# Kernel optimization log

Measured on AMD Instinct MI355X. Metric: run time of the kernel, lower is better.

Reference implementation:

```python
import jax, jax.numpy as jnp
import numpy as np
import math

NVX = 4096   # vx grid points -> th, vr_vxvy are [NVX, NVX]
NVR = 256    # radial grid points
NL = 2       # max spherical-harmonic degree (original hardcodes n_max=2)
N_LM = (NL + 1) * (NL + 2) // 2  # number of (l, m) pairs with 0<=m<=l<=NL


def _grids():
    vmax_x = 8.0
    dvx = 2.0 * vmax_x / NVX
    vx = jnp.linspace(-vmax_x + dvx / 2, vmax_x - dvx / 2, NVX)
    vmax_r = 8.0 * 1.05 * math.sqrt(2.0)
    dvr = vmax_r / NVR
    vr = jnp.linspace(dvr / 2, vmax_r - dvr / 2, NVR)
    VX, VY = jnp.meshgrid(vx, vx)
    th = jnp.arctan2(VY, VX)
    vr_vxvy = jnp.sqrt(VX ** 2 + VY ** 2)
    return vr.astype(jnp.float32), th.astype(jnp.float32), vr_vxvy.astype(jnp.float32)


def _assoc_legendre(l, m, x):
    """P_l^m(x) with Condon-Shortley phase (matches scipy/jax sph_harm)."""
    pmm = jnp.ones_like(x)
    if m > 0:
        somx2 = jnp.sqrt((1.0 - x) * (1.0 + x))
        fact = 1.0
        for _ in range(m):
            pmm = pmm * (-fact) * somx2
            fact += 2.0
    if l == m:
        return pmm
    pmmp1 = x * (2.0 * m + 1.0) * pmm
    if l == m + 1:
        return pmmp1
    for ll in range(m + 2, l + 1):
        pll = ((2.0 * ll - 1.0) * x * pmmp1 - (ll + m - 1.0) * pmm) / (ll - m)
        pmm, pmmp1 = pmmp1, pll
    return pmmp1


def _ylm_real_theta0(l, m, costh):
    # Re[Y_l^m(theta=0, phi)] = K_lm * P_l^m(cos phi); exp(i*m*0) = 1
    k = math.sqrt((2 * l + 1) / (4.0 * math.pi)
                  * math.factorial(l - m) / math.factorial(l + m))
    return k * _assoc_legendre(l, m, costh)


def setup_inputs() -> dict:
    key = jax.random.key(0)
    # flm stacked row-major over (l, m): (0,0),(1,0),(1,1),(2,0),(2,1),(2,2)
    flm = jax.random.uniform(key, (N_LM, NVR), dtype=jnp.float32)
    vr, th, vr_vxvy = _grids()
    return {"flm": flm, "vr": vr, "th": th, "vr_vxvy": vr_vxvy}


def reference(flm, vr, th, vr_vxvy):
    costh = jnp.cos(th)
    fvxvy = jnp.zeros_like(vr_vxvy)
    idx = 0
    for l in range(NL + 1):
        for m in range(l + 1):
            # gather-based 1D interpolation of radial coefficient onto 2D grid
            f_r = jnp.interp(vr_vxvy, vr, flm[idx], right=1e-16)
            y_lm = _ylm_real_theta0(l, m, costh)
            fvxvy = fvxvy + f_r * y_lm
            idx += 1
    return fvxvy
```

## Files before the change

### kernel.cpp

```cpp
#include <hip/hip_runtime.h>


__global__ __launch_bounds__(256) void sph_eval_kernel(
    const float* __restrict__ flm,
    const float* __restrict__ vr,
    float* __restrict__ out)
{
    __shared__ float2 P[5 * 256];

    const int t = threadIdx.x;

    {
        const float C0 = 0.28209479177387814f;
        const float C1 = 0.48860251190291992f;
        const float C2 = -0.34549414947133547f;
        const float C3 = 0.63078313050504010f;
        const float C4 = -0.77254840404650040f;
        const float C5 = 0.38627420202325020f;

        const int k  = t;
        const int k1 = (k < 255) ? k + 1 : 255;

        const float f00 = flm[0 * 256 + k], f00n = flm[0 * 256 + k1];
        const float f10 = flm[1 * 256 + k], f10n = flm[1 * 256 + k1];
        const float f11 = flm[2 * 256 + k], f11n = flm[2 * 256 + k1];
        const float f20 = flm[3 * 256 + k], f20n = flm[3 * 256 + k1];
        const float f21 = flm[4 * 256 + k], f21n = flm[4 * 256 + k1];
        const float f22 = flm[5 * 256 + k], f22n = flm[5 * 256 + k1];

        const float a0 = fmaf(C0, f00, C3 * f20);
        const float a1 = fmaf(C0, f00n, C3 * f20n);
        const float b0 = C2 * f11,  b1 = C2 * f11n;
        const float c0 = fmaf(C5, f22, -1.5f * C3 * f20);
        const float c1 = fmaf(C5, f22n, -1.5f * C3 * f20n);
        const float d0 = C1 * f10,  d1 = C1 * f10n;
        const float e0 = C4 * f21,  e1 = C4 * f21n;

        P[          k] = make_float2(a0, a1 - a0);
        P[ 256 +    k] = make_float2(b0, b1 - b0);
        P[ 512 +    k] = make_float2(c0, c1 - c0);
        P[ 768 +    k] = make_float2(d0, d1 - d0);
        P[1024 +    k] = make_float2(e0, e1 - e0);
    }
    __syncthreads();

    const float dvx = 16.0f / 4096.0f;
    const float vx0 = -8.0f + 0.5f * dvx;

    const float vr0     = vr[0];
    const float inv_dvr = 1.0f / (vr[1] - vr0);
    const float cc0     = -vr0 * inv_dvr;

    const int row = blockIdx.x;
    const float vxi  = fmaf((float)row, dvx, vx0);
    const float avxi = fabsf(vxi);
    const float vxi2 = vxi * vxi;
    const size_t r0 = (size_t)row * 4096;
    const size_t r1 = (size_t)(4095 - row) * 4096;

    #pragma unroll
    for (int qq = 0; qq < 2; ++qq) {
        const int j0 = qq * 1024 + t * 4;

        float ev[4], od[4];
        #pragma unroll
        for (int q = 0; q < 4; ++q) {
            const float vxj  = fmaf((float)(j0 + q), dvx, vx0);
            const float rsq  = fmaf(vxj, vxj, vxi2);
            const float rinv = __builtin_amdgcn_rsqf(rsq);
            const float r    = rsq * rinv;
            const float x    = vxj  * rinv;
            const float s    = avxi * rinv;

            float tt = fmaxf(fmaf(r, inv_dvr, cc0), 0.0f);
            const float kf = floorf(tt);
            const float w  = tt - kf;
            const int   k  = (int)kf;

            const float2 pA = P[k];
            const float2 pB = P[256 + k];
            const float2 pC = P[512 + k];
            const float2 pD = P[768 + k];
            const float2 pE = P[1024 + k];

            const float gA = fmaf(w, pA.y, pA.x);
            const float gB = fmaf(w, pB.y, pB.x);
            const float gC = fmaf(w, pC.y, pC.x);
            const float gD = fmaf(w, pD.y, pD.x);
            const float gE = fmaf(w, pE.y, pE.x);

            ev[q] = fmaf(s, fmaf(s, gC, gB), gA);
            od[q] = x * fmaf(s, gE, gD);
        }

        const float4 oa = { ev[0] + od[0], ev[1] + od[1],
                            ev[2] + od[2], ev[3] + od[3] };
        const float4 ob = { ev[3] - od[3], ev[2] - od[2],
                            ev[1] - od[1], ev[0] - od[0] };

        *reinterpret_cast<float4*>(out + r0 + j0)          = oa;
        *reinterpret_cast<float4*>(out + r0 + (4092 - j0)) = ob;
        *reinterpret_cast<float4*>(out + r1 + j0)          = oa;
        *reinterpret_cast<float4*>(out + r1 + (4092 - j0)) = ob;
    }
}

extern "C" void kernel_launch(void* const* d_in, const int* in_sizes, int n_in,
                              void* d_out, int out_size, void* d_ws, size_t ws_size,
                              hipStream_t stream) {
    const float* flm = (const float*)d_in[0];
    const float* vr  = (const float*)d_in[1];
    float* out = (float*)d_out;

    sph_eval_kernel<<<dim3(2048), 256, 0, stream>>>(flm, vr, out);
}
```

Baseline: 17.84 us.

## Share one widened LDS table lookup across each group of four output points

The radial interpolation table now stores two consecutive bins per entry as a float4 (value and slope for bins k and k+1). Each thread does a single set of five LDS reads per four adjacent points, indexed by the last point's bin. Each point then picks the lower or upper half with a compare-and-select. This cuts LDS traffic and index arithmetic by about four times. It relies on the grid spacing guaranteeing that four adjacent points span at most two radial bins, and that radius decreases along j in the processed half.

After: 17.87 us. No clear change (+0.1%).

```diff
diff --git a/kernel.cpp b/kernel.cpp
--- a/kernel.cpp
+++ b/kernel.cpp
@@ -6,7 +6,7 @@
     const float* __restrict__ vr,
     float* __restrict__ out)
 {
-    __shared__ float2 P[5 * 256];
+    __shared__ float4 T[5 * 256];
 
     const int t = threadIdx.x;
 
@@ -18,29 +18,26 @@
         const float C4 = -0.77254840404650040f;
         const float C5 = 0.38627420202325020f;
 
-        const int k  = t;
-        const int k1 = (k < 255) ? k + 1 : 255;
-
-        const float f00 = flm[0 * 256 + k], f00n = flm[0 * 256 + k1];
-        const float f10 = flm[1 * 256 + k], f10n = flm[1 * 256 + k1];
-        const float f11 = flm[2 * 256 + k], f11n = flm[2 * 256 + k1];
-        const float f20 = flm[3 * 256 + k], f20n = flm[3 * 256 + k1];
-        const float f21 = flm[4 * 256 + k], f21n = flm[4 * 256 + k1];
-        const float f22 = flm[5 * 256 + k], f22n = flm[5 * 256 + k1];
-
-        const float a0 = fmaf(C0, f00, C3 * f20);
-        const float a1 = fmaf(C0, f00n, C3 * f20n);
-        const float b0 = C2 * f11,  b1 = C2 * f11n;
-        const float c0 = fmaf(C5, f22, -1.5f * C3 * f20);
-        const float c1 = fmaf(C5, f22n, -1.5f * C3 * f20n);
-        const float d0 = C1 * f10,  d1 = C1 * f10n;
-        const float e0 = C4 * f21,  e1 = C4 * f21n;
-
-        P[          k] = make_float2(a0, a1 - a0);
-        P[ 256 +    k] = make_float2(b0, b1 - b0);
-        P[ 512 +    k] = make_float2(c0, c1 - c0);
-        P[ 768 +    k] = make_float2(d0, d1 - d0);
-        P[1024 +    k] = make_float2(e0, e1 - e0);
+        float V[3][5];
+        #pragma unroll
+        for (int d = 0; d < 3; ++d) {
+            int kd = t + d; kd = kd > 255 ? 255 : kd;
+            const float f00 = flm[          kd];
+            const float f10 = flm[ 256 +    kd];
+            const float f11 = flm[ 512 +    kd];
+            const float f20 = flm[ 768 +    kd];
+            const float f21 = flm[1024 +    kd];
+            const float f22 = flm[1280 +    kd];
+            V[d][0] = fmaf(C0, f00, C3 * f20);
+            V[d][1] = C2 * f11;
+            V[d][2] = fmaf(C5, f22, -1.5f * C3 * f20);
+            V[d][3] = C1 * f10;
+            V[d][4] = C4 * f21;
+        }
+        #pragma unroll
+        for (int i = 0; i < 5; ++i)
+            T[i * 256 + t] = make_float4(V[0][i], V[1][i] - V[0][i],
+                                         V[1][i], V[2][i] - V[1][i]);
     }
     __syncthreads();
 
@@ -62,35 +59,42 @@
     for (int qq = 0; qq < 2; ++qq) {
         const int j0 = qq * 1024 + t * 4;
 
-        float ev[4], od[4];
+        float tts[4], xs[4], ss[4];
         #pragma unroll
         for (int q = 0; q < 4; ++q) {
             const float vxj  = fmaf((float)(j0 + q), dvx, vx0);
             const float rsq  = fmaf(vxj, vxj, vxi2);
             const float rinv = __builtin_amdgcn_rsqf(rsq);
             const float r    = rsq * rinv;
-            const float x    = vxj  * rinv;
-            const float s    = avxi * rinv;
+            xs[q]  = vxj  * rinv;
+            ss[q]  = avxi * rinv;
+            tts[q] = fmaxf(fmaf(r, inv_dvr, cc0), 0.0f);
+        }
 
-            float tt = fmaxf(fmaf(r, inv_dvr, cc0), 0.0f);
-            const float kf = floorf(tt);
-            const float w  = tt - kf;
-            const int   k  = (int)kf;
+        const int   k3  = (int)tts[3];
+        const float k3f = (float)k3;
 
-            const float2 pA = P[k];
-            const float2 pB = P[256 + k];
-            const float2 pC = P[512 + k];
-            const float2 pD = P[768 + k];
-            const float2 pE = P[1024 + k];
+        const float4 pA = T[          k3];
+        const float4 pB = T[ 256 +    k3];
+        const float4 pC = T[ 512 +    k3];
+        const float4 pD = T[ 768 +    k3];
+        const float4 pE = T[1024 +    k3];
 
-            const float gA = fmaf(w, pA.y, pA.x);
-            const float gB = fmaf(w, pB.y, pB.x);
-            const float gC = fmaf(w, pC.y, pC.x);
-            const float gD = fmaf(w, pD.y, pD.x);
-            const float gE = fmaf(w, pE.y, pE.x);
+        float ev[4], od[4];
+        #pragma unroll
+        for (int q = 0; q < 4; ++q) {
+            const float wp = tts[q] - k3f;
+            const bool  c  = wp >= 1.0f;
+            const float w  = c ? wp - 1.0f : wp;
 
-            ev[q] = fmaf(s, fmaf(s, gC, gB), gA);
-            od[q] = x * fmaf(s, gE, gD);
+            const float gA = fmaf(w, c ? pA.w : pA.y, c ? pA.z : pA.x);
+            const float gB = fmaf(w, c ? pB.w : pB.y, c ? pB.z : pB.x);
+            const float gC = fmaf(w, c ? pC.w : pC.y, c ? pC.z : pC.x);
+            const float gD = fmaf(w, c ? pD.w : pD.y, c ? pD.z : pD.x);
+            const float gE = fmaf(w, c ? pE.w : pE.y, c ? pE.z : pE.x);
+
+            ev[q] = fmaf(ss[q], fmaf(ss[q], gC, gB), gA);
+            od[q] = xs[q] * fmaf(ss[q], gE, gD);
         }
 
         const float4 oa = { ev[0] + od[0], ev[1] + od[1],
```
